# Performance work log

Measured on AMD Instinct MI355X. Metric: run time of the kernel, lower is better.

The kernel has to match this reference:

```python
import jax, jax.numpy as jnp
import numpy as np

N, T, V, C, H = 16, 512, 33, 3, 64
EPS = 1e-5
CONNECTIONS = [(0,1),(1,2),(2,3),(3,7),(0,4),(4,5),(5,6),(6,8),(9,10),(11,12),(11,13),(13,15),(12,14),(14,16),(15,17),(15,19),(15,21),(17,19),(16,18),(16,20),(16,22),(18,20),(11,23),(12,24),(23,24),(23,25),(25,27),(24,26),(26,28),(27,29),(27,31),(29,31),(28,30),(28,32)]


def _adjacency():
    A = np.zeros((V, V), dtype=np.float32)
    for i, j in CONNECTIONS:
        A[i, j] = 1.0
        A[j, i] = 1.0
    A = A + np.eye(V, dtype=np.float32)
    return jnp.asarray(A / A.sum(axis=1, keepdims=True))  # D^{-1} A row-normalization


def setup_inputs() -> dict:
    key = jax.random.key(0)
    ks = iter(jax.random.split(key, 80))
    def nrm(shape, s=0.05):
        return jax.random.normal(next(ks), shape, jnp.float32) * s
    d = {"x": jax.random.normal(next(ks), (N, T, V, C), jnp.float32), "A": _adjacency()}
    def bn(prefix, shape):
        d[prefix + "g"] = 1.0 + nrm(shape, 0.1)
        d[prefix + "b"] = nrm(shape, 0.1)
        d[prefix + "m"] = jnp.zeros(shape, jnp.float32)
        d[prefix + "v"] = jnp.ones(shape, jnp.float32)
    bn("dbn_", (C * V,))
    d["b1_gw"] = nrm((H, C)); d["b1_gb"] = nrm((H,))
    bn("b1_bn1", (H,)); d["b1_tw"] = nrm((H, H, 9)); d["b1_tb"] = nrm((H,)); bn("b1_bn2", (H,))
    d["m_gw"] = nrm((3, H, H)); d["m_gb"] = nrm((3, H))
    bn("m_bn1", (3, H)); d["m_tw"] = nrm((3, H, H, 9)); d["m_tb"] = nrm((3, H)); bn("m_bn2", (3, H))
    d["b5_gw"] = nrm((C, H)); d["b5_gb"] = nrm((C,))
    bn("b5_bn1", (C,)); d["b5_tw"] = nrm((C, C, 9)); d["b5_tb"] = nrm((C,)); bn("b5_bn2", (C,))
    return d


def _bn2d(y, g, b, m, v):
    sh = (1, -1, 1, 1)
    return (y - m.reshape(sh)) * (g.reshape(sh) * jax.lax.rsqrt(v.reshape(sh) + EPS)) + b.reshape(sh)


def _block(y, A, gw, gb, g1, b1, m1, v1, tw, tb, g2, b2, m2, v2, residual):
    res = y if residual else 0.0
    # GraphConv: 1x1 conv (K=1 partition) then joint aggregation with normalized adjacency
    z = jnp.einsum('nctv,oc->notv', y, gw) + gb.reshape(1, -1, 1, 1)
    z = jnp.einsum('nctv,vw->nctw', z, A)
    # TCN: BN -> ReLU -> 9x1 temporal conv (pad 4) -> BN (dropout identity in eval)
    z = jax.nn.relu(_bn2d(z, g1, b1, m1, v1))
    z = jax.lax.conv_general_dilated(z, tw[..., None], (1, 1), [(4, 4), (0, 0)],
                                     dimension_numbers=('NCHW', 'OIHW', 'NCHW')) + tb.reshape(1, -1, 1, 1)
    z = _bn2d(z, g2, b2, m2, v2)
    return jax.nn.relu(z + res)


def _forward(x, A, dbn_g, dbn_b, dbn_m, dbn_v, b1_gw, b1_gb, b1_bn1g, b1_bn1b, b1_bn1m, b1_bn1v, b1_tw, b1_tb, b1_bn2g, b1_bn2b, b1_bn2m, b1_bn2v, m_gw, m_gb, m_bn1g, m_bn1b, m_bn1m, m_bn1v, m_tw, m_tb, m_bn2g, m_bn2b, m_bn2m, m_bn2v, b5_gw, b5_gb, b5_bn1g, b5_bn1b, b5_bn1m, b5_bn1v, b5_tw, b5_tb, b5_bn2g, b5_bn2b, b5_bn2m, b5_bn2v):
    xc = jnp.transpose(x, (0, 3, 1, 2))  # N,C,T,V
    # data_bn: raw view of NCTV contiguous buffer as (N, C*V, T), matching torch .view
    xr = xc.reshape(N, C * V, T)
    xr = (xr - dbn_m[:, None]) * (dbn_g[:, None] * jax.lax.rsqrt(dbn_v[:, None] + EPS)) + dbn_b[:, None]
    y = xr.reshape(N, C, T, V)
    y = _block(y, A, b1_gw, b1_gb, b1_bn1g, b1_bn1b, b1_bn1m, b1_bn1v, b1_tw, b1_tb, b1_bn2g, b1_bn2b, b1_bn2m, b1_bn2v, False)
    for i in range(3):
        y = _block(y, A, m_gw[i], m_gb[i], m_bn1g[i], m_bn1b[i], m_bn1m[i], m_bn1v[i], m_tw[i], m_tb[i], m_bn2g[i], m_bn2b[i], m_bn2m[i], m_bn2v[i], True)
    y = _block(y, A, b5_gw, b5_gb, b5_bn1g, b5_bn1b, b5_bn1m, b5_bn1v, b5_tw, b5_tb, b5_bn2g, b5_bn2b, b5_bn2m, b5_bn2v, False)
    return jnp.transpose(xc + y, (0, 2, 3, 1))  # N,T,V,C


def reference(x, A, dbn_g, dbn_b, dbn_m, dbn_v, b1_gw, b1_gb, b1_bn1g, b1_bn1b, b1_bn1m, b1_bn1v, b1_tw, b1_tb, b1_bn2g, b1_bn2b, b1_bn2m, b1_bn2v, m_gw, m_gb, m_bn1g, m_bn1b, m_bn1m, m_bn1v, m_tw, m_tb, m_bn2g, m_bn2b, m_bn2m, m_bn2v, b5_gw, b5_gb, b5_bn1g, b5_bn1b, b5_bn1m, b5_bn1v, b5_tw, b5_tb, b5_bn2g, b5_bn2b, b5_bn2m, b5_bn2v):
    return _forward(x, A, dbn_g, dbn_b, dbn_m, dbn_v, b1_gw, b1_gb, b1_bn1g, b1_bn1b, b1_bn1m, b1_bn1v, b1_tw, b1_tb, b1_bn2g, b1_bn2b, b1_bn2m, b1_bn2v, m_gw, m_gb, m_bn1g, m_bn1b, m_bn1m, m_bn1v, m_tw, m_tb, m_bn2g, m_bn2b, m_bn2m, m_bn2v, b5_gw, b5_gb, b5_bn1g, b5_bn1b, b5_bn1m, b5_bn1v, b5_tw, b5_tb, b5_bn2g, b5_bn2b, b5_bn2m, b5_bn2v)
```

## Files before the change

### kernel.cpp

```cpp
#include <hip/hip_runtime.h>
#include <hip/hip_bf16.h>


constexpr int N_ = 16, T_ = 512, V_ = 33, C_ = 3, H_ = 64;
constexpr float EPS_ = 1e-5f;

typedef __attribute__((ext_vector_type(8))) short short8;
typedef __attribute__((ext_vector_type(4))) float f32x4;

__device__ inline unsigned short f2bf(float f) {
    union { __hip_bfloat16 h; unsigned short u; } cv;
    cv.h = __float2bfloat16(f);
    return cv.u;
}
__device__ inline float bf2f(unsigned short u) {
    union { unsigned short u; __hip_bfloat16 h; } cv;
    cv.u = u;
    return __bfloat162float(cv.h);
}

__global__ __launch_bounds__(256) void k_prep(
    const float* __restrict__ b1_tw, const float* __restrict__ m_tw,
    const float* __restrict__ b1_gw, const float* __restrict__ m_gw,
    const float* __restrict__ Adj,
    unsigned short* __restrict__ wT_bf, unsigned short* __restrict__ gw_bf,
    unsigned short* __restrict__ ATbf, float* __restrict__ colsum,
    float* __restrict__ gwT_b1)
{
    int idx = blockIdx.x * 256 + threadIdx.x;
    if (idx < 147456) {
        int s = idx / 36864, r = idx % 36864;
        int k = r / 4096, o = (r % 4096) / 64, i = r % 64;
        const float* src = (s == 0) ? b1_tw : (m_tw + (size_t)(s - 1) * 36864);
        wT_bf[idx] = f2bf(src[(o * 64 + i) * 9 + k]);
    } else if (idx < 147456 + 12288) {
        int r = idx - 147456;
        gw_bf[r] = f2bf(m_gw[r]);
    } else if (idx < 147456 + 12288 + 3456) {
        int r = idx - 159744;
        int w = r / 72, vv = r % 72;
        ATbf[r] = (w < 33 && vv < 33) ? f2bf(Adj[vv * 33 + w]) : (unsigned short)0;
    } else if (idx < 147456 + 12288 + 3456 + 48) {
        int w = idx - 163200;
        float s = 0.f;
        if (w < 33)
            for (int vv = 0; vv < 33; ++vv) s += Adj[vv * 33 + w];
        colsum[w] = s;
    } else if (idx < 147456 + 12288 + 3456 + 48 + 192) {
        int r = idx - 163248;
        int c = r / 64, o = r % 64;
        gwT_b1[r] = b1_gw[o * 3 + c];
    }
}

__global__ __launch_bounds__(256) void k_stageA_b1(
    const float* __restrict__ x,
    unsigned short* __restrict__ out,
    const float* __restrict__ Adj,
    const float* __restrict__ gwT,
    const float* __restrict__ gb,
    const float* __restrict__ g1, const float* __restrict__ b1,
    const float* __restrict__ m1, const float* __restrict__ v1,
    const float* __restrict__ dg, const float* __restrict__ db,
    const float* __restrict__ dm, const float* __restrict__ dv)
{
    __shared__ float sy[V_ * 4];
    __shared__ float su[V_ * 68];
    __shared__ float sA[V_ * V_];
    __shared__ float sgwT[3 * 64];

    int nt = blockIdx.x;
    int t = nt & (T_ - 1);
    int tid = threadIdx.x;
    const float* src = x + (size_t)nt * (V_ * 3);
    for (int idx = tid; idx < V_ * 3; idx += 256) {
        int v = idx / 3, c = idx % 3;
        int jj = c * V_ + ((t * V_ + v) >> 9);
        float s = dg[jj] * rsqrtf(dv[jj] + EPS_);
        sy[v * 4 + c] = (src[idx] - dm[jj]) * s + db[jj];
    }
    for (int idx = tid; idx < V_ * V_; idx += 256) sA[idx] = Adj[idx];
    for (int idx = tid; idx < 3 * 64; idx += 256) sgwT[idx] = gwT[idx];
    __syncthreads();

    for (int idx = tid; idx < V_ * 16; idx += 256) {
        int v = idx >> 4, oq = idx & 15, o4 = oq * 4;
        float a0 = gb[o4], a1 = gb[o4 + 1], a2 = gb[o4 + 2], a3 = gb[o4 + 3];
#pragma unroll
        for (int c = 0; c < 3; ++c) {
            float yv = sy[v * 4 + c];
            const float4 w4 = *reinterpret_cast<const float4*>(&sgwT[c * 64 + o4]);
            a0 = fmaf(yv, w4.x, a0); a1 = fmaf(yv, w4.y, a1);
            a2 = fmaf(yv, w4.z, a2); a3 = fmaf(yv, w4.w, a3);
        }
        *reinterpret_cast<float4*>(&su[v * 68 + o4]) = make_float4(a0, a1, a2, a3);
    }
    __syncthreads();

    for (int idx = tid; idx < V_ * 16; idx += 256) {
        int w = idx >> 4, oq = idx & 15, o4 = oq * 4;
        float a0 = 0.f, a1 = 0.f, a2 = 0.f, a3 = 0.f;
        for (int v = 0; v < V_; ++v) {
            float av = sA[v * V_ + w];
            const float4 u4 = *reinterpret_cast<const float4*>(&su[v * 68 + o4]);
            a0 = fmaf(av, u4.x, a0); a1 = fmaf(av, u4.y, a1);
            a2 = fmaf(av, u4.z, a2); a3 = fmaf(av, u4.w, a3);
        }
        float acc[4] = {a0, a1, a2, a3};
        unsigned short r4[4];
#pragma unroll
        for (int j = 0; j < 4; ++j) {
            int o = o4 + j;
            float s = g1[o] * rsqrtf(v1[o] + EPS_);
            float tt = b1[o] - m1[o] * s;
            r4[j] = f2bf(fmaxf(fmaf(acc[j], s, tt), 0.f));
        }
        *reinterpret_cast<ushort4*>(&out[(size_t)nt * (V_ * 64) + w * 64 + o4]) =
            *reinterpret_cast<ushort4*>(r4);
    }
}

__global__ __launch_bounds__(256) void k_stageA_mfma(
    const unsigned short* __restrict__ in,
    unsigned short* __restrict__ out,
    const unsigned short* __restrict__ ATbf,
    const float* __restrict__ colsum,
    const unsigned short* __restrict__ gwbf,
    const float* __restrict__ gb,
    const float* __restrict__ g1, const float* __restrict__ b1,
    const float* __restrict__ m1, const float* __restrict__ v1)
{
    __shared__ unsigned short Ys[4 * 48 * 72];
    __shared__ unsigned short UT[64 * 72];
    __shared__ float cs[48];

    int nt0 = blockIdx.x * 4;
    int tid = threadIdx.x;
    int wv = tid >> 6, lane = tid & 63;
    int l15 = lane & 15, lg = lane >> 4;
    int o = wv * 16 + l15;

    short8 atf[3][2];
#pragma unroll
    for (int mf = 0; mf < 3; ++mf)
#pragma unroll
        for (int kk = 0; kk < 2; ++kk)
            atf[mf][kk] = *reinterpret_cast<const short8*>(
                ATbf + (16 * mf + l15) * 72 + kk * 32 + lg * 8);
    short8 gwf[2];
#pragma unroll
    for (int kk = 0; kk < 2; ++kk)
        gwf[kk] = *reinterpret_cast<const short8*>(gwbf + o * 64 + kk * 32 + lg * 8);

    float gbl = gb[o];
    float s1 = g1[o] * rsqrtf(v1[o] + EPS_);
    float c1 = b1[o] - m1[o] * s1;

    for (int idx = tid; idx < 1056; idx += 256) {
        int j = idx / 264, r = idx % 264;
        int v = r >> 3, cc = r & 7;
        *reinterpret_cast<short8*>(&Ys[(j * 48 + v) * 72 + cc * 8]) =
            *reinterpret_cast<const short8*>(in + ((size_t)(nt0 + j) * V_ + v) * 64 + cc * 8);
    }
    for (int idx = tid; idx < 540; idx += 256) {
        int j = idx / 135, r = idx % 135;
        int v = 33 + r / 9, cc = r % 9;
        short8 z = {};
        *reinterpret_cast<short8*>(&Ys[(j * 48 + v) * 72 + cc * 8]) = z;
    }
    for (int idx = tid; idx < 128; idx += 256) {
        int oo = idx >> 1, cc = idx & 1;
        short8 z = {};
        *reinterpret_cast<short8*>(&UT[oo * 72 + 48 + cc * 8]) = z;
    }
    if (tid < 48) cs[tid] = colsum[tid];
    __syncthreads();

    for (int j = 0; j < 4; ++j) {
#pragma unroll
        for (int mf = 0; mf < 3; ++mf) {
            f32x4 au = {};
#pragma unroll
            for (int kk = 0; kk < 2; ++kk) {
                short8 a = *reinterpret_cast<const short8*>(
                    &Ys[(j * 48 + 16 * mf + l15) * 72 + kk * 32 + lg * 8]);
                au = __builtin_amdgcn_mfma_f32_16x16x32_bf16(a, gwf[kk], au, 0, 0, 0);
            }
            unsigned short pk[4];
            pk[0] = f2bf(au[0]); pk[1] = f2bf(au[1]);
            pk[2] = f2bf(au[2]); pk[3] = f2bf(au[3]);
            *reinterpret_cast<ushort4*>(&UT[o * 72 + 16 * mf + lg * 4]) =
                *reinterpret_cast<ushort4*>(pk);
        }
        __syncthreads();
        short8 bu[2];
#pragma unroll
        for (int kk = 0; kk < 2; ++kk)
            bu[kk] = *reinterpret_cast<const short8*>(&UT[o * 72 + kk * 32 + lg * 8]);
#pragma unroll
        for (int mf2 = 0; mf2 < 3; ++mf2) {
            f32x4 az = {};
#pragma unroll
            for (int kk = 0; kk < 2; ++kk)
                az = __builtin_amdgcn_mfma_f32_16x16x32_bf16(atf[mf2][kk], bu[kk], az, 0, 0, 0);
#pragma unroll
            for (int r = 0; r < 4; ++r) {
                int w = 16 * mf2 + lg * 4 + r;
                if (w < 33) {
                    float val = az[r] + gbl * cs[w];
                    float y = fmaxf(val * s1 + c1, 0.f);
                    out[((size_t)(nt0 + j) * V_ + w) * 64 + o] = f2bf(y);
                }
            }
        }
        __syncthreads();
    }
}

template <bool RES>
__global__ __launch_bounds__(256) void k_stageB_mfma(
    const unsigned short* __restrict__ z,
    unsigned short* __restrict__ out,
    const unsigned short* __restrict__ wbf,
    const float* __restrict__ tb,
    const float* __restrict__ g2, const float* __restrict__ b2,
    const float* __restrict__ m2, const float* __restrict__ vv2)
{
    __shared__ unsigned short sa[2][72 * 64];

    int bx = blockIdx.x, v = blockIdx.y, n = blockIdx.z;
    int base_t0 = bx * 256;
    int tid = threadIdx.x;
    int wv = tid >> 6, lane = tid & 63;
    int l15 = lane & 15, lg = lane >> 4;
    int o = wv * 16 + l15;

    short8 bw[18];
#pragma unroll
    for (int k = 0; k < 9; ++k)
#pragma unroll
        for (int c = 0; c < 2; ++c)
            bw[k * 2 + c] = *reinterpret_cast<const short8*>(
                wbf + ((k * 64 + o) * 64) + c * 32 + lg * 8);

    float s2 = g2[o] * rsqrtf(vv2[o] + EPS_);
    float c2 = (tb[o] - m2[o]) * s2 + b2[o];

    short8 stg[3];

#define LOADJ(jj)                                                             \
    {                                                                         \
        int t0l = base_t0 + (jj) * 64;                                        \
        _Pragma("unroll")                                                     \
        for (int it = 0; it < 3; ++it) {                                      \
            int idx = tid + it * 256;                                         \
            if (idx < 576) {                                                  \
                int r = idx >> 3;                                             \
                int tg = t0l - 4 + r;                                         \
                short8 val = {};                                              \
                if (tg >= 0 && tg < T_)                                       \
                    val = *reinterpret_cast<const short8*>(                   \
                        z + ((size_t)(n * T_ + tg) * V_ + v) * 64 +           \
                        (idx & 7) * 8);                                       \
                stg[it] = val;                                                \
            }                                                                 \
        }                                                                     \
    }

#define WRITEJ(pp)                                                            \
    {                                                                         \
        _Pragma("unroll")                                                     \
        for (int it = 0; it < 3; ++it) {                                      \
            int idx = tid + it * 256;                                         \
            if (idx < 576) {                                                  \
                int r = idx >> 3, cc = idx & 7;                               \
                int slot = cc ^ (r & 7);                                      \
                *reinterpret_cast<short8*>(                                   \
                    reinterpret_cast<char*>(&sa[pp][0]) + r * 128 +           \
                    slot * 16) = stg[it];                                     \
            }                                                                 \
        }                                                                     \
    }

    LOADJ(0);
    WRITEJ(0);
    __syncthreads();

    int p = 0;
    for (int j = 0; j < 4; ++j) {
        if (j < 3) LOADJ(j + 1);

        int t0 = base_t0 + j * 64;

        unsigned short res[16];
        if (RES) {
#pragma unroll
            for (int f = 0; f < 4; ++f)
#pragma unroll
                for (int r = 0; r < 4; ++r) {
                    int t = t0 + f * 16 + lg * 4 + r;
                    res[f * 4 + r] =
                        out[((size_t)(n * T_ + t) * V_ + v) * 64 + o];
                }
        }

        f32x4 acc[4] = {};
        for (int k = 0; k < 9; ++k) {
#pragma unroll
            for (int c = 0; c < 2; ++c) {
                short8 b = bw[k * 2 + c];
#pragma unroll
                for (int f = 0; f < 4; ++f) {
                    int r = f * 16 + l15 + k;
                    int slot = (c * 4 + lg) ^ (r & 7);
                    short8 a = *reinterpret_cast<const short8*>(
                        reinterpret_cast<const char*>(&sa[p][0]) + r * 128 + slot * 16);
                    acc[f] = __builtin_amdgcn_mfma_f32_16x16x32_bf16(a, b, acc[f], 0, 0, 0);
                }
            }
        }

#pragma unroll
        for (int f = 0; f < 4; ++f) {
#pragma unroll
            for (int r = 0; r < 4; ++r) {
                int t = t0 + f * 16 + lg * 4 + r;
                size_t addr = ((size_t)(n * T_ + t) * V_ + v) * 64 + o;
                float zz = acc[f][r] * s2 + c2;
                if (RES) zz += bf2f(res[f * 4 + r]);
                out[addr] = f2bf(fmaxf(zz, 0.f));
            }
        }

        if (j < 3) WRITEJ(p ^ 1);
        __syncthreads();
        p ^= 1;
    }
#undef LOADJ
#undef WRITEJ
}

__global__ __launch_bounds__(256) void k_stageA_b5(
    const unsigned short* __restrict__ in,
    float* __restrict__ out,
    const float* __restrict__ Adj,
    const float* __restrict__ gw,
    const float* __restrict__ gb,
    const float* __restrict__ g1, const float* __restrict__ b1,
    const float* __restrict__ m1, const float* __restrict__ v1)
{
    __shared__ float sy[V_ * 64];
    __shared__ float su[V_ * 4];
    __shared__ float sA[V_ * V_];
    int nt = blockIdx.x;
    int tid = threadIdx.x;
    const unsigned short* src = in + (size_t)nt * (V_ * 64);
    for (int idx = tid; idx < 264; idx += 256) {
        short8 val = *reinterpret_cast<const short8*>(src + idx * 8);
#pragma unroll
        for (int e = 0; e < 8; ++e)
            sy[idx * 8 + e] = bf2f((unsigned short)val[e]);
    }
    for (int idx = tid; idx < V_ * V_; idx += 256) sA[idx] = Adj[idx];
    __syncthreads();
    for (int idx = tid; idx < V_ * 3; idx += 256) {
        int v = idx / 3, o = idx % 3;
        float a = gb[o];
        for (int c = 0; c < 64; ++c) a = fmaf(sy[v * 64 + c], gw[o * 64 + c], a);
        su[v * 4 + o] = a;
    }
    __syncthreads();
    for (int idx = tid; idx < V_ * 3; idx += 256) {
        int w = idx / 3, o = idx % 3;
        float a = 0.f;
        for (int vv = 0; vv < V_; ++vv) a = fmaf(su[vv * 4 + o], sA[vv * V_ + w], a);
        float s = g1[o] * rsqrtf(v1[o] + EPS_);
        float zz = (a - m1[o]) * s + b1[o];
        out[(size_t)nt * (V_ * 3) + w * 3 + o] = fmaxf(zz, 0.f);
    }
}

__global__ __launch_bounds__(256) void k_stageB_b5(
    const float* __restrict__ z5,
    const float* __restrict__ x,
    float* __restrict__ out,
    const float* __restrict__ tw,
    const float* __restrict__ tb,
    const float* __restrict__ g2, const float* __restrict__ b2,
    const float* __restrict__ m2, const float* __restrict__ v2)
{
    int idx = blockIdx.x * 256 + threadIdx.x;
    if (idx >= N_ * T_ * V_) return;
    int v = idx % V_;
    int t = (idx / V_) % T_;
    int n = idx / (V_ * T_);
    float acc0 = tb[0], acc1 = tb[1], acc2 = tb[2];
    for (int k = 0; k < 9; ++k) {
        int tg = t + k - 4;
        if (tg < 0 || tg >= T_) continue;
        const float* zp = &z5[((size_t)(n * T_ + tg) * V_ + v) * 3];
        float zi0 = zp[0], zi1 = zp[1], zi2 = zp[2];
        acc0 = fmaf(tw[0 * 9 + k], zi0, acc0);
        acc0 = fmaf(tw[1 * 9 + k], zi1, acc0);
        acc0 = fmaf(tw[2 * 9 + k], zi2, acc0);
        acc1 = fmaf(tw[3 * 9 + k], zi0, acc1);
        acc1 = fmaf(tw[4 * 9 + k], zi1, acc1);
        acc1 = fmaf(tw[5 * 9 + k], zi2, acc1);
        acc2 = fmaf(tw[6 * 9 + k], zi0, acc2);
        acc2 = fmaf(tw[7 * 9 + k], zi1, acc2);
        acc2 = fmaf(tw[8 * 9 + k], zi2, acc2);
    }
    size_t base = (size_t)idx * 3;
    float a[3] = {acc0, acc1, acc2};
#pragma unroll
    for (int oo = 0; oo < 3; ++oo) {
        float s = g2[oo] * rsqrtf(v2[oo] + EPS_);
        float zz = (a[oo] - m2[oo]) * s + b2[oo];
        out[base + oo] = x[base + oo] + fmaxf(zz, 0.f);
    }
}

extern "C" void kernel_launch(void* const* d_in, const int* in_sizes, int n_in,
                              void* d_out, int out_size, void* d_ws, size_t ws_size,
                              hipStream_t stream) {
    int a = 0;
    const float* x      = (const float*)d_in[a++];
    const float* Adj    = (const float*)d_in[a++];
    const float* dbn_g  = (const float*)d_in[a++];
    const float* dbn_b  = (const float*)d_in[a++];
    const float* dbn_m  = (const float*)d_in[a++];
    const float* dbn_v  = (const float*)d_in[a++];
    const float* b1_gw  = (const float*)d_in[a++];
    const float* b1_gb  = (const float*)d_in[a++];
    const float* b1_bn1g = (const float*)d_in[a++];
    const float* b1_bn1b = (const float*)d_in[a++];
    const float* b1_bn1m = (const float*)d_in[a++];
    const float* b1_bn1v = (const float*)d_in[a++];
    const float* b1_tw  = (const float*)d_in[a++];
    const float* b1_tb  = (const float*)d_in[a++];
    const float* b1_bn2g = (const float*)d_in[a++];
    const float* b1_bn2b = (const float*)d_in[a++];
    const float* b1_bn2m = (const float*)d_in[a++];
    const float* b1_bn2v = (const float*)d_in[a++];
    const float* m_gw   = (const float*)d_in[a++];
    const float* m_gb   = (const float*)d_in[a++];
    const float* m_bn1g = (const float*)d_in[a++];
    const float* m_bn1b = (const float*)d_in[a++];
    const float* m_bn1m = (const float*)d_in[a++];
    const float* m_bn1v = (const float*)d_in[a++];
    const float* m_tw   = (const float*)d_in[a++];
    const float* m_tb   = (const float*)d_in[a++];
    const float* m_bn2g = (const float*)d_in[a++];
    const float* m_bn2b = (const float*)d_in[a++];
    const float* m_bn2m = (const float*)d_in[a++];
    const float* m_bn2v = (const float*)d_in[a++];
    const float* b5_gw  = (const float*)d_in[a++];
    const float* b5_gb  = (const float*)d_in[a++];
    const float* b5_bn1g = (const float*)d_in[a++];
    const float* b5_bn1b = (const float*)d_in[a++];
    const float* b5_bn1m = (const float*)d_in[a++];
    const float* b5_bn1v = (const float*)d_in[a++];
    const float* b5_tw  = (const float*)d_in[a++];
    const float* b5_tb  = (const float*)d_in[a++];
    const float* b5_bn2g = (const float*)d_in[a++];
    const float* b5_bn2b = (const float*)d_in[a++];
    const float* b5_bn2m = (const float*)d_in[a++];
    const float* b5_bn2v = (const float*)d_in[a++];

    char* ws = (char*)d_ws;
    const size_t S_BIG_B  = (size_t)N_ * T_ * V_ * 64 * 2;
    const size_t S_SM_B   = (size_t)N_ * T_ * V_ * 3 * 4;
    unsigned short* B0     = (unsigned short*)(ws);
    unsigned short* B1     = (unsigned short*)(ws + S_BIG_B);
    float*          z5     = (float*)(ws + 2 * S_BIG_B + S_SM_B);
    unsigned short* wT_bf  = (unsigned short*)(ws + 2 * S_BIG_B + 2 * S_SM_B);
    unsigned short* gw_bf  = wT_bf + 147456;
    unsigned short* ATbf   = gw_bf + 12288;
    float*          colsum = (float*)(ATbf + 3456);
    float*          gwT_b1 = colsum + 48;

    k_prep<<<(163440 + 255) / 256, 256, 0, stream>>>(
        b1_tw, m_tw, b1_gw, m_gw, Adj, wT_bf, gw_bf, ATbf, colsum, gwT_b1);

    k_stageA_b1<<<N_ * T_, 256, 0, stream>>>(
        x, B1, Adj, gwT_b1, b1_gb, b1_bn1g, b1_bn1b, b1_bn1m, b1_bn1v,
        dbn_g, dbn_b, dbn_m, dbn_v);
    k_stageB_mfma<false><<<dim3(T_ / 256, V_, N_), 256, 0, stream>>>(
        B1, B0, wT_bf, b1_tb, b1_bn2g, b1_bn2b, b1_bn2m, b1_bn2v);

    for (int i = 0; i < 3; ++i) {
        k_stageA_mfma<<<(N_ * T_) / 4, 256, 0, stream>>>(
            B0, B1, ATbf, colsum, gw_bf + i * 4096, m_gb + i * 64,
            m_bn1g + i * 64, m_bn1b + i * 64, m_bn1m + i * 64, m_bn1v + i * 64);
        k_stageB_mfma<true><<<dim3(T_ / 256, V_, N_), 256, 0, stream>>>(
            B1, B0, wT_bf + (1 + i) * 36864, m_tb + i * 64,
            m_bn2g + i * 64, m_bn2b + i * 64, m_bn2m + i * 64, m_bn2v + i * 64);
    }

    k_stageA_b5<<<N_ * T_, 256, 0, stream>>>(
        B0, z5, Adj, b5_gw, b5_gb, b5_bn1g, b5_bn1b, b5_bn1m, b5_bn1v);
    k_stageB_b5<<<(N_ * T_ * V_ + 255) / 256, 256, 0, stream>>>(
        z5, x, (float*)d_out, b5_tw, b5_tb, b5_bn2g, b5_bn2b, b5_bn2m, b5_bn2v);
}
```

Before: 291.1 us.

## Retile temporal-conv MFMA waves as 2x2 over time and output channels

Changes the wave-to-tile mapping in the stage-B temporal conv kernel. Each wave previously covered all 64 time rows for one 16-channel slice; now a 2x2 grid of waves each covers 32 time rows by 32 output channels. Each LDS A-fragment load now feeds two MFMAs instead of one, halving LDS reads per MFMA. The cost is doubled weight registers (36 short8) per thread, which the added launch_bounds min-blocks hint of 2 may cause to spill or reduce occupancy.

```diff
diff --git a/kernel.cpp b/kernel.cpp
--- a/kernel.cpp
+++ b/kernel.cpp
@@ -218,7 +218,7 @@
 }
 
 template <bool RES>
-__global__ __launch_bounds__(256) void k_stageB_mfma(
+__global__ __launch_bounds__(256, 2) void k_stageB_mfma(
     const unsigned short* __restrict__ z,
     unsigned short* __restrict__ out,
     const unsigned short* __restrict__ wbf,
@@ -231,20 +231,29 @@
     int bx = blockIdx.x, v = blockIdx.y, n = blockIdx.z;
     int base_t0 = bx * 256;
     int tid = threadIdx.x;
-    int wv = tid >> 6, lane = tid & 63;
+    int wave = tid >> 6, lane = tid & 63;
+    int wt = wave >> 1, wo = wave & 1;
     int l15 = lane & 15, lg = lane >> 4;
-    int o = wv * 16 + l15;
-
-    short8 bw[18];
-#pragma unroll
-    for (int k = 0; k < 9; ++k)
-#pragma unroll
-        for (int c = 0; c < 2; ++c)
-            bw[k * 2 + c] = *reinterpret_cast<const short8*>(
-                wbf + ((k * 64 + o) * 64) + c * 32 + lg * 8);
-
-    float s2 = g2[o] * rsqrtf(vv2[o] + EPS_);
-    float c2 = (tb[o] - m2[o]) * s2 + b2[o];
+
+    short8 bw[2][18];
+#pragma unroll
+    for (int s = 0; s < 2; ++s) {
+        int os = (wo * 2 + s) * 16 + l15;
+#pragma unroll
+        for (int k = 0; k < 9; ++k)
+#pragma unroll
+            for (int c = 0; c < 2; ++c)
+                bw[s][k * 2 + c] = *reinterpret_cast<const short8*>(
+                    wbf + ((size_t)(k * 64 + os)) * 64 + c * 32 + lg * 8);
+    }
+
+    float s2c[2], c2c[2];
+#pragma unroll
+    for (int s = 0; s < 2; ++s) {
+        int os = (wo * 2 + s) * 16 + l15;
+        s2c[s] = g2[os] * rsqrtf(vv2[os] + EPS_);
+        c2c[s] = (tb[os] - m2[os]) * s2c[s] + b2[os];
+    }
 
     short8 stg[3];
 
@@ -292,43 +301,53 @@
 
         int t0 = base_t0 + j * 64;
 
-        unsigned short res[16];
+        unsigned short res[2][8];
         if (RES) {
 #pragma unroll
-            for (int f = 0; f < 4; ++f)
-#pragma unroll
-                for (int r = 0; r < 4; ++r) {
-                    int t = t0 + f * 16 + lg * 4 + r;
-                    res[f * 4 + r] =
-                        out[((size_t)(n * T_ + t) * V_ + v) * 64 + o];
-                }
-        }
-
-        f32x4 acc[4] = {};
+            for (int s = 0; s < 2; ++s) {
+                int os = (wo * 2 + s) * 16 + l15;
+#pragma unroll
+                for (int f = 0; f < 2; ++f)
+#pragma unroll
+                    for (int r = 0; r < 4; ++r) {
+                        int t = t0 + wt * 32 + f * 16 + lg * 4 + r;
+                        res[s][f * 4 + r] =
+                            out[((size_t)(n * T_ + t) * V_ + v) * 64 + os];
+                    }
+            }
+        }
+
+        f32x4 acc[2][2] = {};
         for (int k = 0; k < 9; ++k) {
 #pragma unroll
             for (int c = 0; c < 2; ++c) {
-                short8 b = bw[k * 2 + c];
-#pragma unroll
-                for (int f = 0; f < 4; ++f) {
-                    int r = f * 16 + l15 + k;
+                short8 b0 = bw[0][k * 2 + c];
+                short8 b1v = bw[1][k * 2 + c];
+#pragma unroll
+                for (int f = 0; f < 2; ++f) {
+                    int r = wt * 32 + f * 16 + l15 + k;
                     int slot = (c * 4 + lg) ^ (r & 7);
                     short8 a = *reinterpret_cast<const short8*>(
                         reinterpret_cast<const char*>(&sa[p][0]) + r * 128 + slot * 16);
-                    acc[f] = __builtin_amdgcn_mfma_f32_16x16x32_bf16(a, b, acc[f], 0, 0, 0);
+                    acc[0][f] = __builtin_amdgcn_mfma_f32_16x16x32_bf16(a, b0, acc[0][f], 0, 0, 0);
+                    acc[1][f] = __builtin_amdgcn_mfma_f32_16x16x32_bf16(a, b1v, acc[1][f], 0, 0, 0);
                 }
             }
         }
 
 #pragma unroll
-        for (int f = 0; f < 4; ++f) {
-#pragma unroll
-            for (int r = 0; r < 4; ++r) {
-                int t = t0 + f * 16 + lg * 4 + r;
-                size_t addr = ((size_t)(n * T_ + t) * V_ + v) * 64 + o;
-                float zz = acc[f][r] * s2 + c2;
-                if (RES) zz += bf2f(res[f * 4 + r]);
-                out[addr] = f2bf(fmaxf(zz, 0.f));
+        for (int s = 0; s < 2; ++s) {
+            int os = (wo * 2 + s) * 16 + l15;
+#pragma unroll
+            for (int f = 0; f < 2; ++f) {
+#pragma unroll
+                for (int r = 0; r < 4; ++r) {
+                    int t = t0 + wt * 32 + f * 16 + lg * 4 + r;
+                    size_t addr = ((size_t)(n * T_ + t) * V_ + v) * 64 + os;
+                    float zz = acc[s][f][r] * s2c[s] + c2c[s];
+                    if (RES) zz += bf2f(res[s][f * 4 + r]);
+                    out[addr] = f2bf(fmaxf(zz, 0.f));
+                }
             }
         }
 
```

Measured after the change: 333.9 us. 1.15x slower.
